# Kernel optimization log

Measured on AMD Instinct MI355X. Metric: run time of the kernel, lower is better.

The kernel has to match this reference:

```python
import jax, jax.numpy as jnp
import numpy as np

OUT = 260        # RESIZE_OUTPUT_IMAGES_SHAPE
TH = 0.8         # OD_SCORE_TH
PCT = 1.0        # INTERNAL_PERCENTAGE_IMAGE_TOTAKE
N_BOXES = 10     # loop bound in original call()
TAPS = 6         # lanczos3 support (radius 3 -> 6 taps, antialias=False)


def _lanczos_taps(src, size):
    """src: (OUT,) float sample coords in crop-local space; size: traced int crop size.
    Returns clamped tap indices (OUT,6) and normalized lanczos3 weights (OUT,6)."""
    base = jnp.floor(src).astype(jnp.int32) - 2
    taps = base[:, None] + jnp.arange(TAPS, dtype=jnp.int32)          # (OUT,6)
    d = src[:, None] - taps.astype(src.dtype)
    w = jnp.where(jnp.abs(d) < 3.0, jnp.sinc(d) * jnp.sinc(d / 3.0), 0.0)
    w = w / jnp.sum(w, axis=1, keepdims=True)
    idx = jnp.clip(taps, 0, size - 1)
    return idx, w


def _crop_resize(img, box):
    """img: (H,W,3). box: (4,) normalized [ymin,xmin,ymax,xmax] -> (OUT,OUT,3).
    Matches tf.image.resize lanczos3 (antialias=False): half-pixel centers, clamped edges."""
    H, W = img.shape[0], img.shape[1]
    y0 = (box[0] * H).astype(jnp.int32)
    x0 = (box[1] * W).astype(jnp.int32)
    y1 = (box[2] * H).astype(jnp.int32)
    x1 = (box[3] * W).astype(jnp.int32)
    ch = jnp.maximum(y1 - y0, 1)
    cw = jnp.maximum(x1 - x0, 1)
    o = jnp.arange(OUT, dtype=img.dtype)
    src_h = (o + 0.5) * (ch.astype(img.dtype) / OUT) - 0.5
    src_w = (o + 0.5) * (cw.astype(img.dtype) / OUT) - 0.5
    idx_h, w_h = _lanczos_taps(src_h, ch)
    idx_w, w_w = _lanczos_taps(src_w, cw)
    idx_h = idx_h + y0
    idx_w = idx_w + x0
    # vertical pass: gather 6 row taps per output row, reduce -> (OUT, W, 3)
    rows = jnp.einsum('pa,pawc->pwc', w_h, img[idx_h])
    # horizontal pass: gather 6 col taps per output col, reduce -> (OUT, OUT, 3)
    out = jnp.einsum('qb,pqbc->pqc', w_w, rows[:, idx_w])
    return out


def setup_inputs() -> dict:
    key = jax.random.key(0)
    k1, k2, k3, k4 = jax.random.split(key, 4)
    # scores: first 10 mostly above threshold, rest below
    s_hi = 0.85 + 0.15 * jax.random.uniform(k1, (N_BOXES,), dtype=jnp.float32)
    s_lo = 0.8 * jax.random.uniform(k2, (100 - N_BOXES,), dtype=jnp.float32)
    od_scores = jnp.concatenate([s_hi, s_lo])
    # bboxes (ymin,xmin,ymax,xmax) with guaranteed positive crop sizes
    u = jax.random.uniform(k3, (100, 4), dtype=jnp.float32)
    od_bboxes = jnp.stack([u[:, 0] * 0.45, u[:, 1] * 0.45,
                           0.55 + 0.45 * u[:, 2], 0.55 + 0.45 * u[:, 3]], axis=1)
    image = jax.random.normal(k4, (1, 2048, 2048, 3), dtype=jnp.float32)
    return {"od_scores": od_scores, "od_bboxes": od_bboxes, "image": image}


def reference(od_scores, od_bboxes, image):
    img = image[0]                           # (H,W,3)
    b10 = od_bboxes[:N_BOXES]
    s10 = od_scores[:N_BOXES]
    valid = ((od_scores[0] >= TH) & (s10 >= TH)
             & (b10[:, 1] >= 0.5 - PCT / 2.0)
             & (b10[:, 3] <= 0.5 + PCT / 2.0))
    crops = jax.vmap(lambda b: _crop_resize(img, b))(b10)   # (10,OUT,OUT,3)
    return crops * valid[:, None, None, None].astype(img.dtype)
```

## Files before the change

kernel.cpp:

```cpp
#include <hip/hip_runtime.h>
#include <math.h>

#define OUT 260
#define TAPS 6
#define IMG_H 2048
#define IMG_W 2048
#define ROW_F (IMG_W * 3)
#define NB 10
#define TH 0.8f
#define QB 65
#define SEGS 4
#define LDSF 1600

__device__ __forceinline__ float sincf(float x) {
    if (x == 0.0f) return 1.0f;
    float px = 3.14159265358979323846f * x;
    return __sinf(px) / px;
}


__global__ __launch_bounds__(320) void tables_kernel(
    const float* __restrict__ scores, const float* __restrict__ boxes,
    float* __restrict__ htab, float* __restrict__ vtab)
{
    const int box = blockIdx.x;
    const float b0 = boxes[box * 4 + 0];
    const float b1 = boxes[box * 4 + 1];
    const float b2 = boxes[box * 4 + 2];
    const float b3 = boxes[box * 4 + 3];

    const int y0 = (int)(b0 * (float)IMG_H);
    const int x0 = (int)(b1 * (float)IMG_W);
    const int y1 = (int)(b2 * (float)IMG_H);
    const int x1 = (int)(b3 * (float)IMG_W);
    const int ch = max(y1 - y0, 1);
    const int cw = max(x1 - x0, 1);

    const bool valid = (scores[0] >= TH) && (scores[box] >= TH)
                    && (b1 >= 0.0f) && (b3 <= 1.0f);
    const float vmask = valid ? 1.0f : 0.0f;

    const int t = threadIdx.x;
    if (t >= OUT) return;

    {
        const float src = ((float)t + 0.5f) * ((float)cw / (float)OUT) - 0.5f;
        const int base = (int)floorf(src) - 2;
        float w[TAPS]; int id[TAPS];
        float s = 0.0f;
        #pragma unroll
        for (int k = 0; k < TAPS; ++k) {
            const float d = src - (float)(base + k);
            const float wv = (fabsf(d) < 3.0f) ? sincf(d) * sincf(d * (1.0f / 3.0f)) : 0.0f;
            w[k] = wv; s += wv;
            int tt = base + k; tt = tt < 0 ? 0 : tt; tt = tt > cw - 1 ? cw - 1 : tt;
            id[k] = (x0 + tt) * 3;
        }
        const float inv = 1.0f / s;
        float* h = htab + ((size_t)(box * OUT + t) << 4);
        int*   hi = (int*)h;
        #pragma unroll
        for (int k = 0; k < TAPS; ++k) { h[k] = w[k] * inv; hi[8 + k] = id[k]; }
        h[6] = 0.0f; h[7] = 0.0f; hi[14] = 0; hi[15] = 0;
    }

    {
        const float src = ((float)t + 0.5f) * ((float)ch / (float)OUT) - 0.5f;
        const int base = (int)floorf(src) - 2;
        float w[TAPS]; int id[TAPS];
        float s = 0.0f;
        #pragma unroll
        for (int k = 0; k < TAPS; ++k) {
            const float d = src - (float)(base + k);
            const float wv = (fabsf(d) < 3.0f) ? sincf(d) * sincf(d * (1.0f / 3.0f)) : 0.0f;
            w[k] = wv; s += wv;
            int tt = base + k; tt = tt < 0 ? 0 : tt; tt = tt > ch - 1 ? ch - 1 : tt;
            id[k] = tt + y0;
        }
        const float inv = vmask / s;
        float* v = vtab + ((size_t)(box * OUT + t) << 4);
        int*   vi = (int*)v;
        #pragma unroll
        for (int k = 0; k < TAPS; ++k) { v[k] = w[k] * inv; vi[8 + k] = id[k]; }
        v[6] = 0.0f; v[7] = 0.0f; vi[14] = 0; vi[15] = 0;
    }
}

__global__ __launch_bounds__(64) void crop_resize_seg(
    const float* __restrict__ img,
    const float* __restrict__ htab,
    const float* __restrict__ vtab,
    float* __restrict__ out)
{
    const int seg = blockIdx.x;
    const int p   = blockIdx.y;
    const int box = blockIdx.z;
    const int q0  = seg * QB;

    const float* vrec = vtab + ((size_t)(box * OUT + p) << 4);
    const int*   vi   = (const int*)vrec;
    float wh[TAPS]; int rows[TAPS];
    #pragma unroll
    for (int k = 0; k < TAPS; ++k) { wh[k] = vrec[k]; rows[k] = vi[8 + k]; }

    const int* hi_first = (const int*)(htab + ((size_t)(box * OUT + q0) << 4));
    const int* hi_last  = (const int*)(htab + ((size_t)(box * OUT + q0 + QB - 1) << 4));
    const int start_f = hi_first[8] & ~3;
    const int n_f     = ((hi_last[13] + 3) - start_f + 3) & ~3;

    __shared__ float lds[LDSF];

    {
        const float* r0 = img + (size_t)rows[0] * ROW_F + start_f;
        const float* r1 = img + (size_t)rows[1] * ROW_F + start_f;
        const float* r2 = img + (size_t)rows[2] * ROW_F + start_f;
        const float* r3 = img + (size_t)rows[3] * ROW_F + start_f;
        const float* r4 = img + (size_t)rows[4] * ROW_F + start_f;
        const float* r5 = img + (size_t)rows[5] * ROW_F + start_f;

        for (int f = threadIdx.x * 4; f < n_f; f += 64 * 4) {
            const float4 v0 = *(const float4*)(r0 + f);
            const float4 v1 = *(const float4*)(r1 + f);
            const float4 v2 = *(const float4*)(r2 + f);
            const float4 v3 = *(const float4*)(r3 + f);
            const float4 v4 = *(const float4*)(r4 + f);
            const float4 v5 = *(const float4*)(r5 + f);
            float4 acc;
            acc.x = wh[0]*v0.x + wh[1]*v1.x + wh[2]*v2.x + wh[3]*v3.x + wh[4]*v4.x + wh[5]*v5.x;
            acc.y = wh[0]*v0.y + wh[1]*v1.y + wh[2]*v2.y + wh[3]*v3.y + wh[4]*v4.y + wh[5]*v5.y;
            acc.z = wh[0]*v0.z + wh[1]*v1.z + wh[2]*v2.z + wh[3]*v3.z + wh[4]*v4.z + wh[5]*v5.z;
            acc.w = wh[0]*v0.w + wh[1]*v1.w + wh[2]*v2.w + wh[3]*v3.w + wh[4]*v4.w + wh[5]*v5.w;
            *(float4*)(lds + f) = acc;
        }
    }
    __syncthreads();

    for (int qi = threadIdx.x; qi < QB; qi += 64) {
        const int q = q0 + qi;
        const float* h  = htab + ((size_t)(box * OUT + q) << 4);
        const int*   hi = (const int*)h;
        float a0 = 0.0f, a1 = 0.0f, a2 = 0.0f;
        #pragma unroll
        for (int k = 0; k < TAPS; ++k) {
            const float w  = h[k];
            const int   li = hi[8 + k] - start_f;
            a0 = fmaf(w, lds[li + 0], a0);
            a1 = fmaf(w, lds[li + 1], a1);
            a2 = fmaf(w, lds[li + 2], a2);
        }
        const size_t o = (((size_t)box * OUT + p) * OUT + q) * 3;
        out[o + 0] = a0;
        out[o + 1] = a1;
        out[o + 2] = a2;
    }
}

__global__ __launch_bounds__(256) void crop_resize_fallback(
    const float* __restrict__ scores, const float* __restrict__ boxes,
    const float* __restrict__ img, float* __restrict__ out)
{
    const int p = blockIdx.x, box = blockIdx.y;
    const float b0 = boxes[box*4+0], b1 = boxes[box*4+1];
    const float b2 = boxes[box*4+2], b3 = boxes[box*4+3];
    const int y0 = (int)(b0*(float)IMG_H), x0 = (int)(b1*(float)IMG_W);
    const int y1 = (int)(b2*(float)IMG_H), x1 = (int)(b3*(float)IMG_W);
    const int ch = max(y1-y0,1), cw = max(x1-x0,1);
    const bool valid = (scores[0]>=TH)&&(scores[box]>=TH)&&(b1>=0.0f)&&(b3<=1.0f);
    const float vmask = valid?1.0f:0.0f;
    float wh[TAPS]; int ih[TAPS];
    {
        const float src = ((float)p+0.5f)*((float)ch/(float)OUT)-0.5f;
        const int base = (int)floorf(src)-2;
        float s = 0.0f;
        #pragma unroll
        for (int a = 0; a < TAPS; ++a) {
            const float d = src-(float)(base+a);
            const float w = (fabsf(d)<3.0f)?sincf(d)*sincf(d*(1.0f/3.0f)):0.0f;
            wh[a]=w; s+=w;
            int t=base+a; t=t<0?0:t; t=t>ch-1?ch-1:t; ih[a]=t+y0;
        }
        const float inv = 1.0f/s;
        #pragma unroll
        for (int a = 0; a < TAPS; ++a) wh[a]*=inv;
    }
    const int start_f = (x0*3)&~3;
    const int end_f = (x0+cw)*3;
    const int n_f = end_f-start_f;
    __shared__ float lds[6152];
    {
        const float* r0 = img+(size_t)ih[0]*ROW_F+start_f;
        const float* r1 = img+(size_t)ih[1]*ROW_F+start_f;
        const float* r2 = img+(size_t)ih[2]*ROW_F+start_f;
        const float* r3 = img+(size_t)ih[3]*ROW_F+start_f;
        const float* r4 = img+(size_t)ih[4]*ROW_F+start_f;
        const float* r5 = img+(size_t)ih[5]*ROW_F+start_f;
        for (int f = threadIdx.x*4; f < n_f; f += 256*4) {
            const float4 v0=*(const float4*)(r0+f), v1=*(const float4*)(r1+f);
            const float4 v2=*(const float4*)(r2+f), v3=*(const float4*)(r3+f);
            const float4 v4=*(const float4*)(r4+f), v5=*(const float4*)(r5+f);
            float4 acc;
            acc.x=wh[0]*v0.x+wh[1]*v1.x+wh[2]*v2.x+wh[3]*v3.x+wh[4]*v4.x+wh[5]*v5.x;
            acc.y=wh[0]*v0.y+wh[1]*v1.y+wh[2]*v2.y+wh[3]*v3.y+wh[4]*v4.y+wh[5]*v5.y;
            acc.z=wh[0]*v0.z+wh[1]*v1.z+wh[2]*v2.z+wh[3]*v3.z+wh[4]*v4.z+wh[5]*v5.z;
            acc.w=wh[0]*v0.w+wh[1]*v1.w+wh[2]*v2.w+wh[3]*v3.w+wh[4]*v4.w+wh[5]*v5.w;
            *(float4*)(lds+f)=acc;
        }
    }
    __syncthreads();
    const float wscale = (float)cw/(float)OUT;
    for (int q = threadIdx.x; q < OUT; q += 256) {
        const float src = ((float)q+0.5f)*wscale-0.5f;
        const int basew = (int)floorf(src)-2;
        float ww[TAPS]; float s = 0.0f;
        #pragma unroll
        for (int k = 0; k < TAPS; ++k) {
            const float d = src-(float)(basew+k);
            const float w = (fabsf(d)<3.0f)?sincf(d)*sincf(d*(1.0f/3.0f)):0.0f;
            ww[k]=w; s+=w;
        }
        const float inv = 1.0f/s;
        float a0=0,a1=0,a2=0;
        #pragma unroll
        for (int k = 0; k < TAPS; ++k) {
            int t=basew+k; t=t<0?0:t; t=t>cw-1?cw-1:t;
            const int hb=(x0+t)*3-start_f;
            a0=fmaf(ww[k],lds[hb+0],a0);
            a1=fmaf(ww[k],lds[hb+1],a1);
            a2=fmaf(ww[k],lds[hb+2],a2);
        }
        const float m = vmask*inv;
        const size_t o = (((size_t)box*OUT+p)*OUT+q)*3;
        out[o+0]=a0*m; out[o+1]=a1*m; out[o+2]=a2*m;
    }
}

extern "C" void kernel_launch(void* const* d_in, const int* in_sizes, int n_in,
                              void* d_out, int out_size, void* d_ws, size_t ws_size,
                              hipStream_t stream) {
    const float* scores = (const float*)d_in[0];
    const float* boxes  = (const float*)d_in[1];
    const float* img    = (const float*)d_in[2];
    float* out = (float*)d_out;

    const size_t tab_bytes = (size_t)NB * OUT * 16 * sizeof(float);
    if (ws_size < 2 * tab_bytes) {
        crop_resize_fallback<<<dim3(OUT, NB), dim3(256), 0, stream>>>(scores, boxes, img, out);
        return;
    }
    float* htab = (float*)d_ws;
    float* vtab = (float*)((char*)d_ws + tab_bytes);

    tables_kernel<<<dim3(NB), dim3(320), 0, stream>>>(scores, boxes, htab, vtab);
    crop_resize_seg<<<dim3(SEGS, OUT, NB), dim3(64), 0, stream>>>(img, htab, vtab, out);
}
```

Measured before the change: 113.6 us.

## Compute two output rows per block sharing overlapping vertical tap rows

Each block now produces a pair of adjacent output rows, loading the union of their vertical tap rows once and accumulating both weighted sums, so overlapping source rows are read from global memory once instead of twice. The tables kernel stores each row's tap base so the pair offset can be computed. Column segments shrink to 32 outputs across 9 segments, and the two halves of the 64-thread block each handle one row in the horizontal pass. This adds register pressure from the 14-entry weight and index arrays and a runtime-bounded tap loop.

```diff
diff --git a/kernel.cpp b/kernel.cpp
--- a/kernel.cpp
+++ b/kernel.cpp
@@ -8,9 +8,10 @@
 #define ROW_F (IMG_W * 3)
 #define NB 10
 #define TH 0.8f
-#define QB 65
-#define SEGS 4
-#define LDSF 1600
+#define SEGS 9
+#define QB 32
+#define LROW 800
+#define MAXM 14
 
 __device__ __forceinline__ float sincf(float x) {
     if (x == 0.0f) return 1.0f;
@@ -82,73 +83,89 @@
         int*   vi = (int*)v;
         #pragma unroll
         for (int k = 0; k < TAPS; ++k) { v[k] = w[k] * inv; vi[8 + k] = id[k]; }
-        v[6] = 0.0f; v[7] = 0.0f; vi[14] = 0; vi[15] = 0;
-    }
-}
-
-__global__ __launch_bounds__(64) void crop_resize_seg(
+        v[6] = 0.0f; v[7] = 0.0f; vi[14] = base; vi[15] = 0;
+    }
+}
+
+__global__ __launch_bounds__(64) void crop_resize_pair(
     const float* __restrict__ img,
     const float* __restrict__ htab,
     const float* __restrict__ vtab,
     float* __restrict__ out)
 {
     const int seg = blockIdx.x;
-    const int p   = blockIdx.y;
+    const int py  = blockIdx.y;
     const int box = blockIdx.z;
     const int q0  = seg * QB;
-
-    const float* vrec = vtab + ((size_t)(box * OUT + p) << 4);
-    const int*   vi   = (const int*)vrec;
-    float wh[TAPS]; int rows[TAPS];
+    const int qcount = min(QB, OUT - q0);
+    const int p0 = 2 * py;
+
+    const float* v0 = vtab + ((size_t)(box * OUT + p0) << 4);
+    const float* v1 = vtab + ((size_t)(box * OUT + p0 + 1) << 4);
+    const int* vi0 = (const int*)v0;
+    const int* vi1 = (const int*)v1;
+
+    int dlt = vi1[14] - vi0[14];
+    dlt = dlt < 0 ? 0 : (dlt > MAXM - TAPS ? MAXM - TAPS : dlt);
+    const int m = dlt + TAPS;
+
+    float wa[MAXM], wb[MAXM];
+    int   rowi[MAXM];
     #pragma unroll
-    for (int k = 0; k < TAPS; ++k) { wh[k] = vrec[k]; rows[k] = vi[8 + k]; }
+    for (int j = 0; j < MAXM; ++j) {
+        const float wA = (j < TAPS) ? v0[j] : 0.0f;
+        const int jb = j - dlt;
+        const float wB = (jb >= 0 && jb < TAPS) ? v1[jb] : 0.0f;
+        wa[j] = wA; wb[j] = wB;
+        rowi[j] = (j < TAPS) ? vi0[8 + j] : vi1[8 + ((jb < 0) ? 0 : (jb > 5 ? 5 : jb))];
+    }
 
     const int* hi_first = (const int*)(htab + ((size_t)(box * OUT + q0) << 4));
-    const int* hi_last  = (const int*)(htab + ((size_t)(box * OUT + q0 + QB - 1) << 4));
+    const int* hi_last  = (const int*)(htab + ((size_t)(box * OUT + q0 + qcount - 1) << 4));
     const int start_f = hi_first[8] & ~3;
     const int n_f     = ((hi_last[13] + 3) - start_f + 3) & ~3;
 
-    __shared__ float lds[LDSF];
-
-    {
-        const float* r0 = img + (size_t)rows[0] * ROW_F + start_f;
-        const float* r1 = img + (size_t)rows[1] * ROW_F + start_f;
-        const float* r2 = img + (size_t)rows[2] * ROW_F + start_f;
-        const float* r3 = img + (size_t)rows[3] * ROW_F + start_f;
-        const float* r4 = img + (size_t)rows[4] * ROW_F + start_f;
-        const float* r5 = img + (size_t)rows[5] * ROW_F + start_f;
-
-        for (int f = threadIdx.x * 4; f < n_f; f += 64 * 4) {
-            const float4 v0 = *(const float4*)(r0 + f);
-            const float4 v1 = *(const float4*)(r1 + f);
-            const float4 v2 = *(const float4*)(r2 + f);
-            const float4 v3 = *(const float4*)(r3 + f);
-            const float4 v4 = *(const float4*)(r4 + f);
-            const float4 v5 = *(const float4*)(r5 + f);
-            float4 acc;
-            acc.x = wh[0]*v0.x + wh[1]*v1.x + wh[2]*v2.x + wh[3]*v3.x + wh[4]*v4.x + wh[5]*v5.x;
-            acc.y = wh[0]*v0.y + wh[1]*v1.y + wh[2]*v2.y + wh[3]*v3.y + wh[4]*v4.y + wh[5]*v5.y;
-            acc.z = wh[0]*v0.z + wh[1]*v1.z + wh[2]*v2.z + wh[3]*v3.z + wh[4]*v4.z + wh[5]*v5.z;
-            acc.w = wh[0]*v0.w + wh[1]*v1.w + wh[2]*v2.w + wh[3]*v3.w + wh[4]*v4.w + wh[5]*v5.w;
-            *(float4*)(lds + f) = acc;
-        }
+    __shared__ float lds[2 * LROW];
+
+    for (int f = threadIdx.x * 4; f < n_f; f += 64 * 4) {
+        float4 a0 = make_float4(0.f, 0.f, 0.f, 0.f);
+        float4 a1 = make_float4(0.f, 0.f, 0.f, 0.f);
+        #pragma unroll
+        for (int j = 0; j < TAPS; ++j) {
+            const float4 v = *(const float4*)(img + (size_t)rowi[j] * ROW_F + start_f + f);
+            a0.x = fmaf(wa[j], v.x, a0.x); a0.y = fmaf(wa[j], v.y, a0.y);
+            a0.z = fmaf(wa[j], v.z, a0.z); a0.w = fmaf(wa[j], v.w, a0.w);
+            a1.x = fmaf(wb[j], v.x, a1.x); a1.y = fmaf(wb[j], v.y, a1.y);
+            a1.z = fmaf(wb[j], v.z, a1.z); a1.w = fmaf(wb[j], v.w, a1.w);
+        }
+        for (int j = TAPS; j < m; ++j) {
+            const float4 v = *(const float4*)(img + (size_t)rowi[j] * ROW_F + start_f + f);
+            a1.x = fmaf(wb[j], v.x, a1.x); a1.y = fmaf(wb[j], v.y, a1.y);
+            a1.z = fmaf(wb[j], v.z, a1.z); a1.w = fmaf(wb[j], v.w, a1.w);
+        }
+        *(float4*)(lds + f) = a0;
+        *(float4*)(lds + LROW + f) = a1;
     }
     __syncthreads();
 
-    for (int qi = threadIdx.x; qi < QB; qi += 64) {
+    const int t    = threadIdx.x;
+    const int sel  = t >> 5;
+    const int qi   = t & 31;
+    if (qi < qcount) {
         const int q = q0 + qi;
         const float* h  = htab + ((size_t)(box * OUT + q) << 4);
         const int*   hi = (const int*)h;
+        const float* l  = lds + sel * LROW;
         float a0 = 0.0f, a1 = 0.0f, a2 = 0.0f;
         #pragma unroll
         for (int k = 0; k < TAPS; ++k) {
             const float w  = h[k];
             const int   li = hi[8 + k] - start_f;
-            a0 = fmaf(w, lds[li + 0], a0);
-            a1 = fmaf(w, lds[li + 1], a1);
-            a2 = fmaf(w, lds[li + 2], a2);
-        }
-        const size_t o = (((size_t)box * OUT + p) * OUT + q) * 3;
+            a0 = fmaf(w, l[li + 0], a0);
+            a1 = fmaf(w, l[li + 1], a1);
+            a2 = fmaf(w, l[li + 2], a2);
+        }
+        const size_t o = (((size_t)box * OUT + (p0 + sel)) * OUT + q) * 3;
         out[o + 0] = a0;
         out[o + 1] = a1;
         out[o + 2] = a2;
@@ -195,14 +212,14 @@
         const float* r4 = img+(size_t)ih[4]*ROW_F+start_f;
         const float* r5 = img+(size_t)ih[5]*ROW_F+start_f;
         for (int f = threadIdx.x*4; f < n_f; f += 256*4) {
-            const float4 v0=*(const float4*)(r0+f), v1=*(const float4*)(r1+f);
-            const float4 v2=*(const float4*)(r2+f), v3=*(const float4*)(r3+f);
-            const float4 v4=*(const float4*)(r4+f), v5=*(const float4*)(r5+f);
+            const float4 u0=*(const float4*)(r0+f), u1=*(const float4*)(r1+f);
+            const float4 u2=*(const float4*)(r2+f), u3=*(const float4*)(r3+f);
+            const float4 u4=*(const float4*)(r4+f), u5=*(const float4*)(r5+f);
             float4 acc;
-            acc.x=wh[0]*v0.x+wh[1]*v1.x+wh[2]*v2.x+wh[3]*v3.x+wh[4]*v4.x+wh[5]*v5.x;
-            acc.y=wh[0]*v0.y+wh[1]*v1.y+wh[2]*v2.y+wh[3]*v3.y+wh[4]*v4.y+wh[5]*v5.y;
-            acc.z=wh[0]*v0.z+wh[1]*v1.z+wh[2]*v2.z+wh[3]*v3.z+wh[4]*v4.z+wh[5]*v5.z;
-            acc.w=wh[0]*v0.w+wh[1]*v1.w+wh[2]*v2.w+wh[3]*v3.w+wh[4]*v4.w+wh[5]*v5.w;
+            acc.x=wh[0]*u0.x+wh[1]*u1.x+wh[2]*u2.x+wh[3]*u3.x+wh[4]*u4.x+wh[5]*u5.x;
+            acc.y=wh[0]*u0.y+wh[1]*u1.y+wh[2]*u2.y+wh[3]*u3.y+wh[4]*u4.y+wh[5]*u5.y;
+            acc.z=wh[0]*u0.z+wh[1]*u1.z+wh[2]*u2.z+wh[3]*u3.z+wh[4]*u4.z+wh[5]*u5.z;
+            acc.w=wh[0]*u0.w+wh[1]*u1.w+wh[2]*u2.w+wh[3]*u3.w+wh[4]*u4.w+wh[5]*u5.w;
             *(float4*)(lds+f)=acc;
         }
     }
@@ -228,9 +245,9 @@
             a1=fmaf(ww[k],lds[hb+1],a1);
             a2=fmaf(ww[k],lds[hb+2],a2);
         }
-        const float m = vmask*inv;
+        const float mfac = vmask*inv;
         const size_t o = (((size_t)box*OUT+p)*OUT+q)*3;
-        out[o+0]=a0*m; out[o+1]=a1*m; out[o+2]=a2*m;
+        out[o+0]=a0*mfac; out[o+1]=a1*mfac; out[o+2]=a2*mfac;
     }
 }
 
@@ -251,5 +268,5 @@
     float* vtab = (float*)((char*)d_ws + tab_bytes);
 
     tables_kernel<<<dim3(NB), dim3(320), 0, stream>>>(scores, boxes, htab, vtab);
-    crop_resize_seg<<<dim3(SEGS, OUT, NB), dim3(64), 0, stream>>>(img, htab, vtab, out);
-}
+    crop_resize_pair<<<dim3(SEGS, OUT / 2, NB), dim3(64), 0, stream>>>(img, htab, vtab, out);
+}
```

After: 119.2 us. +5.0%, slower.
